# Performance work log

Measured on AMD Instinct MI355X. Metric: run time of the kernel, lower is better.

The kernel has to match this reference:

```python
import jax, jax.numpy as jnp
import numpy as np

N_NODES = 20000
N_EDGES = 320000
N_GRAPHS = 200
N_LAYERS = 2
TOWERS = 5
F_IN = 75        # divide_input=False -> each tower sees the full 75-dim input
F_OUT = 15       # out_channels // towers = 75 // 5
EDGE_DIM = 50
POST_IN = (4 * 3 + 1) * F_IN  # 4 aggregators * 3 scalers + self = 975
EPS_STD = 1e-5
EPS_BN = 1e-5


def setup_inputs() -> dict:
    key = jax.random.key(0)
    ks = jax.random.split(key, 16)
    x_idx = jax.random.randint(ks[0], (N_NODES,), 0, 10000)
    edge_index = jax.random.randint(ks[1], (2, N_EDGES), 0, N_NODES)
    edge_attr_idx = jax.random.randint(ks[2], (N_EDGES,), 0, 100)
    batch_idx = jnp.sort(jax.random.randint(ks[3], (N_NODES,), 0, N_GRAPHS))

    def g(k, shp, fan):
        return jax.random.normal(k, shp, jnp.float32) * np.float32(1.0 / np.sqrt(fan))

    inp = dict(
        x_idx=x_idx, edge_index=edge_index, edge_attr_idx=edge_attr_idx, batch_idx=batch_idx,
        node_emb=g(ks[4], (10000, F_IN), 1.0),
        edge_emb=g(ks[5], (100, EDGE_DIM), 1.0),
        W_edge=g(ks[6], (N_LAYERS, EDGE_DIM, F_IN), EDGE_DIM),
        b_edge=jnp.zeros((N_LAYERS, F_IN), jnp.float32),
        W_pre=g(ks[7], (N_LAYERS, TOWERS, 3 * F_IN, F_IN), 3 * F_IN),
        b_pre=jnp.zeros((N_LAYERS, TOWERS, F_IN), jnp.float32),
        W_post=g(ks[8], (N_LAYERS, TOWERS, POST_IN, F_OUT), POST_IN),
        b_post=jnp.zeros((N_LAYERS, TOWERS, F_OUT), jnp.float32),
        W_lin=g(ks[9], (N_LAYERS, F_IN, F_IN), F_IN),
        b_lin=jnp.zeros((N_LAYERS, F_IN), jnp.float32),
        bn_gamma=jnp.ones((N_LAYERS, F_IN), jnp.float32),
        bn_beta=jnp.zeros((N_LAYERS, F_IN), jnp.float32),
        W1=g(ks[10], (75, 50), 75), b1=jnp.zeros((50,), jnp.float32),
        W2=g(ks[11], (50, 25), 50), b2=jnp.zeros((25,), jnp.float32),
        W3=g(ks[12], (25, 1), 25), b3=jnp.zeros((1,), jnp.float32),
    )
    return inp


def reference(x_idx, edge_index, edge_attr_idx, batch_idx,
              node_emb, edge_emb, W_edge, b_edge, W_pre, b_pre,
              W_post, b_post, W_lin, b_lin, bn_gamma, bn_beta,
              W1, b1, W2, b2, W3, b3):
    src, dst = edge_index[0], edge_index[1]  # flow source_to_target: aggregate at dst
    x = node_emb[x_idx]                      # [N, 75]
    e_raw = edge_emb[edge_attr_idx]          # [E, 50]

    # in-degree based scalers (PNA); avg log-degree from this graph's degree histogram
    deg = jax.ops.segment_sum(jnp.ones((N_EDGES,), jnp.float32), dst, num_segments=N_NODES)
    avg_log = jnp.mean(jnp.log(deg + 1.0))
    deg_c = jnp.maximum(deg, 1.0)
    amp = (jnp.log(deg_c + 1.0) / avg_log)[:, None, None]
    att = (avg_log / jnp.log(deg_c + 1.0))[:, None, None]
    has_in = (deg > 0.0)[:, None, None]
    inv_deg = (1.0 / deg_c)[:, None, None]

    for l in range(N_LAYERS):
        # edge encoder (shared across towers)
        e = e_raw @ W_edge[l] + b_edge[l]                            # [E, 75]
        # message: since divide_input=False all towers see the same concat input
        h = jnp.concatenate([x[dst], x[src], e], axis=-1)            # [E, 225]
        m = jnp.einsum('ec,tcf->etf', h, W_pre[l]) + b_pre[l]        # [E, T, 75]
        # multi-aggregator reduction at dst
        mean = jax.ops.segment_sum(m, dst, num_segments=N_NODES) * inv_deg
        mean_sq = jax.ops.segment_sum(m * m, dst, num_segments=N_NODES) * inv_deg
        std = jnp.sqrt(jax.nn.relu(mean_sq - mean * mean) + EPS_STD)
        mn = jnp.where(has_in, jax.ops.segment_min(m, dst, num_segments=N_NODES), 0.0)
        mx = jnp.where(has_in, jax.ops.segment_max(m, dst, num_segments=N_NODES), 0.0)
        aggr = jnp.concatenate([mean, mn, mx, std], axis=-1)         # [N, T, 300]
        # degree scalers: identity, amplification, attenuation
        out = jnp.concatenate([aggr, aggr * amp, aggr * att], axis=-1)  # [N, T, 900]
        # update: concat self features, per-tower post MLP, then shared lin
        xt = jnp.broadcast_to(x[:, None, :], (N_NODES, TOWERS, F_IN))
        h2 = jnp.concatenate([xt, out], axis=-1)                     # [N, T, 975]
        y = jnp.einsum('ntc,tcf->ntf', h2, W_post[l]) + b_post[l]    # [N, T, 15]
        y = y.reshape(N_NODES, TOWERS * F_OUT) @ W_lin[l] + b_lin[l] # [N, 75]
        # BatchNorm (training-mode batch stats, biased variance) + ReLU
        mu = jnp.mean(y, axis=0)
        var = jnp.mean((y - mu) ** 2, axis=0)
        y = (y - mu) * jax.lax.rsqrt(var + EPS_BN) * bn_gamma[l] + bn_beta[l]
        x = jax.nn.relu(y)

    pooled = jax.ops.segment_sum(x, batch_idx, num_segments=N_GRAPHS)  # [G, 75]
    h = jax.nn.relu(pooled @ W1 + b1)
    h = jax.nn.relu(h @ W2 + b2)
    return h @ W3 + b3                                               # [G, 1]
```

## Files before the change

### kernel.cpp

```cpp
#include <hip/hip_runtime.h>
#include <hip/hip_bf16.h>
#include <math.h>

#define NN 20000
#define NE 320000
#define NG 200
#define FI 75
#define NT 5
#define FO 15
#define CH 375
#define PI 975
#define SMS 1608

typedef __attribute__((ext_vector_type(8))) short v8s;
typedef __attribute__((ext_vector_type(4))) float v4f;

__device__ __forceinline__ unsigned short f2bfu(float v) {
  __hip_bfloat16 h = __float2bfloat16(v);
  return *reinterpret_cast<unsigned short*>(&h);
}
__device__ __forceinline__ float uif(unsigned u) { return __uint_as_float(u); }

__global__ __launch_bounds__(256) void k_mega1(
    const int* __restrict__ xidx, const float* __restrict__ emb, float* __restrict__ x,
    const int* __restrict__ dstp, int* __restrict__ deg,
    const float* __restrict__ eemb, const float* __restrict__ W_edge,
    const float* __restrict__ b_edge, float* __restrict__ te,
    const float* __restrict__ W_pre, float* __restrict__ WAs,
    const float* __restrict__ W_post, float* __restrict__ V,
    const float* __restrict__ b_post, const float* __restrict__ W_lin,
    const float* __restrict__ b_lin, float* __restrict__ bc) {
  __shared__ float S[FI * 16];
  int b = blockIdx.x, tid = threadIdx.x;
  if (b < 5860) {
    int i = b * 256 + tid;
    if (i < NN * FI) {
      int n = i / FI, f = i - n * FI;
      x[i] = emb[xidx[n] * FI + f];
    }
  } else if (b < 7110) {
    int e = (b - 5860) * 256 + tid;
    if (e < NE) atomicAdd(&deg[dstp[e]], 1);
  } else if (b < 7310) {
    int la = b - 7110;
    int l = la / 100, a = la - l * 100;
    int f = tid;
    if (f < FI) {
      float acc = b_edge[l * FI + f];
      for (int j = 0; j < 50; ++j)
        acc = fmaf(eemb[a * 50 + j], W_edge[(l * 50 + j) * FI + f], acc);
      te[la * FI + f] = acc;
    }
  } else if (b < 7530) {
    int i = (b - 7310) * 256 + tid;
    if (i < 2 * FI * CH) {
      int c = i % CH;
      int k = (i / CH) % FI;
      int l = i / (CH * FI);
      int t = c / FI, f = c - t * FI;
      WAs[i] = W_pre[((size_t)(l * NT + t) * 225 + FI + k) * FI + f];
    }
  } else if (b < 7560) {
    int bid = b - 7530;
    int g = bid % 3;
    int lt = bid / 3;
    for (int idx = tid; idx < FI * 16; idx += 256) {
      int q = idx >> 4, f = idx & 15;
      float v = 0.f;
      if (f < FO) {
        const float* wb = W_post + (size_t)lt * PI * FO;
        int rowb = FI + g * 300 + q;
        v = wb[rowb * FO + f] + wb[(rowb + FI) * FO + f] + wb[(rowb + 2 * FI) * FO + f];
      }
      S[idx] = v;
    }
    __syncthreads();
    for (int idx = tid; idx < FI * 16; idx += 256) {
      int j = idx >> 4, f = idx & 15;
      float acc = 0.f;
      const float* wr = W_pre + ((size_t)lt * 225 + j) * FI;
      for (int q = 0; q < FI; ++q) acc = fmaf(wr[q], S[q * 16 + f], acc);
      V[((size_t)bid * FI + j) * 16 + f] = acc;
    }
  } else {
    int l = b - 7560;
    int g = tid;
    if (g < FI) {
      float acc = b_lin[l * FI + g];
      for (int j = 0; j < FI; ++j)
        acc = fmaf(b_post[l * FI + j], W_lin[(l * FI + j) * FI + g], acc);
      bc[l * 76 + g] = acc;
    }
  }
}

__global__ __launch_bounds__(1024) void k_mega2(
    const int* __restrict__ deg, int* __restrict__ off, int* __restrict__ cur,
    float* __restrict__ avglog,
    const float* __restrict__ te, const float* __restrict__ W_pre,
    const float* __restrict__ b_pre, unsigned short* __restrict__ tm,
    const float* __restrict__ W_post, const float* __restrict__ V,
    unsigned short* __restrict__ Bp,
    const float* __restrict__ WAs, unsigned short* __restrict__ Bxs,
    const float* __restrict__ W_lin, unsigned short* __restrict__ Blin) {
  __shared__ float red[1024];
  int b = blockIdx.x, t = threadIdx.x;
  if (b == 0) {
    int* wsum = (int*)red;
    int base = t * 20;
    int loc[20];
    int s = 0;
#pragma unroll
    for (int j = 0; j < 20; ++j) {
      int i = base + j;
      int v = (i < NN) ? deg[i] : 0;
      loc[j] = s;
      s += v;
    }
    int lane = t & 63, w = t >> 6;
    int inc = s;
    for (int o = 1; o < 64; o <<= 1) {
      int u = __shfl_up(inc, o, 64);
      if (lane >= o) inc += u;
    }
    if (lane == 63) wsum[w] = inc;
    __syncthreads();
    if (t == 0) {
      int a = 0;
#pragma unroll
      for (int k = 0; k < 16; ++k) { int v = wsum[k]; wsum[k] = a; a += v; }
    }
    __syncthreads();
    int tex = wsum[w] + inc - s;
#pragma unroll
    for (int j = 0; j < 20; ++j) {
      int i = base + j;
      if (i < NN) { int e = tex + loc[j]; off[i] = e; cur[i] = e; }
    }
    if (t == 1023) off[NN] = tex + s;
  } else if (b == 1) {
    float s = 0.f;
    for (int i = t; i < NN; i += 1024) s += logf((float)deg[i] + 1.f);
    red[t] = s;
    __syncthreads();
    for (int o = 512; o > 0; o >>= 1) {
      if (t < o) red[t] += red[t + o];
      __syncthreads();
    }
    if (t == 0) avglog[0] = red[0] / (float)NN;
  } else if (b < 77) {
    int idx = (b - 2) * 1024 + t;
    if (idx < 76800) {
      int la = idx / 384, c = idx - la * 384;
      int l = la / 100;
      float acc = 0.f;
      if (c < CH) {
        int tt = c / FI, f = c - tt * FI;
        acc = b_pre[(l * NT + tt) * FI + f];
        const float* ter = te + la * FI;
        for (int k = 0; k < FI; ++k)
          acc = fmaf(ter[k], W_pre[((size_t)(l * NT + tt) * 225 + 150 + k) * FI + f], acc);
      }
      tm[(size_t)la * 384 + c] = f2bfu(acc);
    }
  } else if (b < 302) {
    int i = (b - 77) * 1024 + t;
    if (i < 230400) {
      int j = i & 7;
      int lane = (i >> 3) & 63;
      int rem = i >> 9;
      int kb = rem % 15; rem /= 15;
      int g = rem % 3; rem /= 3;
      int tt = rem % 5;
      int l = rem / 5;
      int k = kb * 32 + (lane >> 4) * 8 + j;
      int f = lane & 15;
      float w = 0.f;
      if (f < FO) {
        int lt = l * NT + tt;
        if (k < 300) {
          int a = k / 75, ch = k - a * 75;
          w = W_post[((size_t)lt * PI + FI + g * 300 + a * 75 + ch) * FO + f];
        } else if (k >= 320 && k < 395) {
          w = V[(((size_t)(lt * 3 + g)) * FI + (k - 320)) * 16 + f];
        } else if (k >= 395 && k < 470 && g == 0) {
          w = W_post[((size_t)lt * PI + (k - 395)) * FO + f];
        }
      }
      Bp[i] = f2bfu(w);
    }
  } else if (b < 374) {
    int i = (b - 302) * 1024 + t;
    if (i < 73728) {
      int j = i & 7;
      int lane = (i >> 3) & 63;
      int rem = i >> 9;
      int nt = rem % 24; rem /= 24;
      int kb = rem % 3;
      int l = rem / 3;
      int k = kb * 32 + (lane >> 4) * 8 + j;
      int n = nt * 16 + (lane & 15);
      float w = 0.f;
      if (k < FI && n < CH) w = WAs[(size_t)l * FI * CH + k * CH + n];
      Bxs[i] = f2bfu(w);
    }
  } else {
    int i = (b - 374) * 1024 + t;
    if (i < 15360) {
      int j = i & 7;
      int lane = (i >> 3) & 63;
      int rem = i >> 9;
      int nt = rem % 5; rem /= 5;
      int kb = rem % 3;
      int l = rem / 3;
      int k = kb * 32 + (lane >> 4) * 8 + j;
      int f = nt * 16 + (lane & 15);
      float w = 0.f;
      if (k < FI && f < FI) w = W_lin[(size_t)l * FI * FI + k * FI + f];
      Blin[i] = f2bfu(w);
    }
  }
}

__global__ __launch_bounds__(256) void k_mega3(
    const int* __restrict__ srcp, const int* __restrict__ dstp,
    const int* __restrict__ attr, int* __restrict__ cur, int2* __restrict__ csr,
    const int* __restrict__ deg, const float* __restrict__ avglog,
    float* __restrict__ amp, float* __restrict__ att, float* __restrict__ inv) {
  int b = blockIdx.x, t = threadIdx.x;
  if (b < 1250) {
    int e = b * 256 + t;
    if (e < NE) {
      int pos = atomicAdd(&cur[dstp[e]], 1);
      csr[pos] = make_int2(srcp[e], attr[e]);
    }
  } else {
    int i = (b - 1250) * 256 + t;
    if (i < NN) {
      float dc = fmaxf((float)deg[i], 1.f);
      float ld = logf(dc + 1.f);
      float av = avglog[0];
      amp[i] = ld / av;
      att[i] = av / ld;
      inv[i] = 1.f / dc;
    }
  }
}

__global__ __launch_bounds__(256) void k_gemm_xs(const float* __restrict__ x,
                                                 const unsigned short* __restrict__ BxsL,
                                                 unsigned short* __restrict__ xsb,
                                                 const int* __restrict__ deg,
                                                 unsigned short* __restrict__ xh,
                                                 float* __restrict__ bnsum) {
  int tid = threadIdx.x;
  if (blockIdx.y == 1) {
    if (blockIdx.x == 0 && tid < 150) bnsum[tid] = 0.f;
    for (int i = blockIdx.x * 256 + tid; i < NN * 160; i += 625 * 256) {
      int r = i / 160, k = i - r * 160;
      float v = 0.f;
      if (k < FI) v = x[(size_t)r * FI + k] * ((deg[r] > 0) ? 1.f : 0.f);
      else if (k < 150) v = x[(size_t)r * FI + k - FI];
      xh[i] = f2bfu(v);
    }
    return;
  }
  __shared__ unsigned short As[32 * 104];
  __shared__ unsigned short Os[32 * 384];
  int m0 = blockIdx.x * 32;
  for (int i = tid; i < 32 * 104; i += 256) {
    int r = i / 104, k = i - r * 104;
    As[i] = (k < FI) ? f2bfu(x[(size_t)(m0 + r) * FI + k]) : 0;
  }
  __syncthreads();
  int lane = tid & 63, w = tid >> 6;
  int m16 = lane & 15, quad = lane >> 4;
  v4f acc0[6], acc1[6];
#pragma unroll
  for (int nt = 0; nt < 6; ++nt) {
    acc0[nt] = {0.f, 0.f, 0.f, 0.f};
    acc1[nt] = {0.f, 0.f, 0.f, 0.f};
  }
  const unsigned short* arow0 = As + m16 * 104 + quad * 8;
  const unsigned short* arow1 = As + (16 + m16) * 104 + quad * 8;
#pragma unroll
  for (int kb = 0; kb < 3; ++kb) {
    v8s a0 = *(const v8s*)(arow0 + kb * 32);
    v8s a1 = *(const v8s*)(arow1 + kb * 32);
#pragma unroll
    for (int nt = 0; nt < 6; ++nt) {
      v8s bf = *(const v8s*)(BxsL + ((size_t)(kb * 24 + w * 6 + nt) * 64 + lane) * 8);
      acc0[nt] = __builtin_amdgcn_mfma_f32_16x16x32_bf16(a0, bf, acc0[nt], 0, 0, 0);
      acc1[nt] = __builtin_amdgcn_mfma_f32_16x16x32_bf16(a1, bf, acc1[nt], 0, 0, 0);
    }
  }
#pragma unroll
  for (int nt = 0; nt < 6; ++nt) {
    int col = w * 96 + nt * 16 + m16;
#pragma unroll
    for (int r = 0; r < 4; ++r) {
      Os[(quad * 4 + r) * 384 + col] = f2bfu(acc0[nt][r]);
      Os[(16 + quad * 4 + r) * 384 + col] = f2bfu(acc1[nt][r]);
    }
  }
  __syncthreads();
  uint4* dst = (uint4*)(xsb + (size_t)m0 * 384);
  const uint4* src = (const uint4*)Os;
  for (int i = tid; i < 1536; i += 256) dst[i] = src[i];
}

__global__ __launch_bounds__(1024) void k_aggpost(
    const unsigned short* __restrict__ xs, const int2* __restrict__ csr,
    const int* __restrict__ off, const float* __restrict__ inv_deg,
    const unsigned short* __restrict__ tm, const unsigned short* __restrict__ xh,
    const unsigned short* __restrict__ Bp, const float* __restrict__ amp,
    const float* __restrict__ att, const unsigned short* __restrict__ BlinL,
    const float* __restrict__ bcL, float* __restrict__ yout,
    float* __restrict__ bnsum) {
  __shared__ __align__(16) unsigned short sm[16 * SMS];
  __shared__ __align__(16) unsigned short zs[16 * 96];
  __shared__ float ysum[FI], ysq[FI];
  int tid = threadIdx.x;
  int wv = tid >> 6, lane = tid & 63;
  int rel0 = blockIdx.x * 16;
  int n = rel0 + wv;
  if (tid < FI) { ysum[tid] = 0.f; ysq[tid] = 0.f; }
  for (int idx = tid; idx < 1600; idx += 1024) {
    int h = idx / 100, pp = idx - h * 100;
    int t = pp / 20, cc = pp - t * 20;
    sm[h * SMS + t * 320 + 300 + cc] = 0;
  }
  for (int i = tid; i < 16 * 21; i += 1024) {
    int r = i / 21, k = 75 + i - r * 21;
    zs[r * 96 + k] = 0;
  }
  if (n < NN) {
    int c0 = lane * 6;
    int o0 = off[n], o1 = off[n + 1];
    float s[6], q[6], mn[6], mx[6];
#pragma unroll
    for (int j = 0; j < 6; ++j) {
      s[j] = 0.f; q[j] = 0.f; mn[j] = INFINITY; mx[j] = -INFINITY;
    }
    auto proc = [&](uint3 xv, uint3 tv) {
      unsigned xa[3] = {xv.x, xv.y, xv.z};
      unsigned ta[3] = {tv.x, tv.y, tv.z};
#pragma unroll
      for (int j = 0; j < 3; ++j) {
        float z0 = uif(xa[j] << 16) + uif(ta[j] << 16);
        float z1 = uif(xa[j] & 0xffff0000u) + uif(ta[j] & 0xffff0000u);
        s[2 * j] += z0; q[2 * j] = fmaf(z0, z0, q[2 * j]);
        mn[2 * j] = fminf(mn[2 * j], z0); mx[2 * j] = fmaxf(mx[2 * j], z0);
        s[2 * j + 1] += z1; q[2 * j + 1] = fmaf(z1, z1, q[2 * j + 1]);
        mn[2 * j + 1] = fminf(mn[2 * j + 1], z1); mx[2 * j + 1] = fmaxf(mx[2 * j + 1], z1);
      }
    };
    int i = o0;
    for (; i + 4 <= o1; i += 4) {
      int2 e0 = csr[i], e1 = csr[i + 1], e2 = csr[i + 2], e3 = csr[i + 3];
      uint3 x0 = *(const uint3*)(xs + (size_t)e0.x * 384 + c0);
      uint3 t0 = *(const uint3*)(tm + (size_t)e0.y * 384 + c0);
      uint3 x1 = *(const uint3*)(xs + (size_t)e1.x * 384 + c0);
      uint3 t1 = *(const uint3*)(tm + (size_t)e1.y * 384 + c0);
      uint3 x2 = *(const uint3*)(xs + (size_t)e2.x * 384 + c0);
      uint3 t2 = *(const uint3*)(tm + (size_t)e2.y * 384 + c0);
      uint3 x3 = *(const uint3*)(xs + (size_t)e3.x * 384 + c0);
      uint3 t3 = *(const uint3*)(tm + (size_t)e3.y * 384 + c0);
      proc(x0, t0); proc(x1, t1); proc(x2, t2); proc(x3, t3);
    }
    for (; i < o1; ++i) {
      int2 e0 = csr[i];
      uint3 x0 = *(const uint3*)(xs + (size_t)e0.x * 384 + c0);
      uint3 t0 = *(const uint3*)(tm + (size_t)e0.y * 384 + c0);
      proc(x0, t0);
    }
    float inv = inv_deg[n];
    bool empty = (o1 == o0);
    unsigned short* srow = sm + wv * SMS;
#pragma unroll
    for (int j = 0; j < 6; ++j) {
      int c = c0 + j;
      if (c < CH) {
        float me = s[j] * inv;
        float sd = sqrtf(fmaxf(q[j] * inv - me * me, 0.f) + 1e-5f);
        float mnv = empty ? 0.f : mn[j];
        float mxv = empty ? 0.f : mx[j];
        int t = c / 75, ch = c - t * 75;
        unsigned short* bb = srow + t * 320;
        bb[ch] = f2bfu(me);
        bb[75 + ch] = f2bfu(mnv);
        bb[150 + ch] = f2bfu(mxv);
        bb[225 + ch] = f2bfu(sd);
      }
    }
  } else {
    uint* rowz = (uint*)(sm + wv * SMS);
    for (int idx2 = lane; idx2 < SMS / 2; idx2 += 64) rowz[idx2] = 0;
  }
  __syncthreads();
  int m16 = lane & 15, quad = lane >> 4;
  if (wv < NT) {
    int tw = wv;
    const unsigned short* arow = sm + m16 * SMS + tw * 320 + quad * 8;
    const unsigned short* xrow = xh + (size_t)(rel0 + m16) * 160 + quad * 8;
    const unsigned short* bp = Bp + ((size_t)tw * 3 * 15 * 64) * 8 + lane * 8;
    v4f a0 = {0.f, 0.f, 0.f, 0.f}, a1 = a0, a2 = a0;
#pragma unroll
    for (int kb = 0; kb < 15; ++kb) {
      v8s av = *(const v8s*)((kb < 10) ? (arow + kb * 32) : (xrow + (kb - 10) * 32));
      const unsigned short* bb = bp + (size_t)kb * 512;
      v8s b0 = *(const v8s*)(bb);
      v8s b1 = *(const v8s*)(bb + 15 * 512);
      v8s b2 = *(const v8s*)(bb + 30 * 512);
      a0 = __builtin_amdgcn_mfma_f32_16x16x32_bf16(av, b0, a0, 0, 0, 0);
      a1 = __builtin_amdgcn_mfma_f32_16x16x32_bf16(av, b1, a1, 0, 0, 0);
      a2 = __builtin_amdgcn_mfma_f32_16x16x32_bf16(av, b2, a2, 0, 0, 0);
    }
    int f = m16;
    if (f < FO) {
      int relZ = quad * 4;
#pragma unroll
      for (int r = 0; r < 4; ++r) {
        int nd = rel0 + relZ + r;
        int ndc = (nd < NN) ? nd : (NN - 1);
        float zz = a0[r] + amp[ndc] * a1[r] + att[ndc] * a2[r];
        zs[(relZ + r) * 96 + tw * FO + f] = f2bfu(zz);
      }
    }
  }
  __syncthreads();
  if (wv < NT) {
    int tw = wv;
    v4f acc2 = {0.f, 0.f, 0.f, 0.f};
#pragma unroll
    for (int kb = 0; kb < 3; ++kb) {
      v8s av = *(const v8s*)(zs + m16 * 96 + quad * 8 + kb * 32);
      v8s bl = *(const v8s*)(BlinL + ((size_t)(kb * 5 + tw) * 64 + lane) * 8);
      acc2 = __builtin_amdgcn_mfma_f32_16x16x32_bf16(av, bl, acc2, 0, 0, 0);
    }
    int fcol = tw * 16 + m16;
    if (fcol < FI) {
      float bcf = bcL[fcol];
      int nb = rel0 + quad * 4;
#pragma unroll
      for (int r = 0; r < 4; ++r) {
        int nd = nb + r;
        if (nd < NN) {
          float v = acc2[r] + bcf;
          yout[(size_t)nd * FI + fcol] = v;
          atomicAdd(&ysum[fcol], v);
          atomicAdd(&ysq[fcol], v * v);
        }
      }
    }
  }
  __syncthreads();
  if (tid < FI) {
    atomicAdd(&bnsum[tid], ysum[tid]);
    atomicAdd(&bnsum[FI + tid], ysq[tid]);
  }
}

__global__ __launch_bounds__(256) void k_bnfinapply(const float* __restrict__ y,
    const float* __restrict__ bnsum, const float* __restrict__ gamL,
    const float* __restrict__ betL, float* __restrict__ xo,
    const int* __restrict__ batch, float* __restrict__ pooled, int dopool) {
  __shared__ float sc[150];
  int tid = threadIdx.x;
  if (tid < FI) {
    float mu = bnsum[tid] / (float)NN;
    float var = bnsum[FI + tid] / (float)NN - mu * mu;
    float scl = gamL[tid] * rsqrtf(var + 1e-5f);
    sc[tid] = scl;
    sc[FI + tid] = betL[tid] - mu * scl;
  }
  if (!dopool) {
    for (int i = blockIdx.x * 256 + tid; i < NG * FI; i += gridDim.x * 256)
      pooled[i] = 0.f;
  }
  __syncthreads();
  int stride = gridDim.x * 256;
  for (int i = blockIdx.x * 256 + tid; i < NN * FI; i += stride) {
    int n = i / FI, f = i - n * FI;
    float v = fmaxf(fmaf(y[i], sc[f], sc[FI + f]), 0.f);
    xo[i] = v;
    if (dopool) atomicAdd(&pooled[batch[n] * FI + f], v);
  }
}

__global__ void k_head(const float* __restrict__ pooled, const float* __restrict__ W1,
                       const float* __restrict__ b1, const float* __restrict__ W2,
                       const float* __restrict__ b2, const float* __restrict__ W3,
                       const float* __restrict__ b3, float* __restrict__ out) {
  __shared__ float p[FI], h1[50], h2[25];
  int g = blockIdx.x, t = threadIdx.x;
  for (int i = t; i < FI; i += 64) p[i] = pooled[g * FI + i];
  __syncthreads();
  if (t < 50) {
    float a = b1[t];
    for (int j = 0; j < FI; ++j) a = fmaf(p[j], W1[j * 50 + t], a);
    h1[t] = fmaxf(a, 0.f);
  }
  __syncthreads();
  if (t < 25) {
    float a = b2[t];
    for (int j = 0; j < 50; ++j) a = fmaf(h1[j], W2[j * 25 + t], a);
    h2[t] = fmaxf(a, 0.f);
  }
  __syncthreads();
  if (t == 0) {
    float a = b3[0];
    for (int j = 0; j < 25; ++j) a = fmaf(h2[j], W3[j], a);
    out[g] = a;
  }
}

extern "C" void kernel_launch(void* const* d_in, const int* in_sizes, int n_in,
                              void* d_out, int out_size, void* d_ws, size_t ws_size,
                              hipStream_t stream) {
  const int* x_idx = (const int*)d_in[0];
  const int* eidx  = (const int*)d_in[1];
  const int* srcp  = eidx;
  const int* dstp  = eidx + NE;
  const int* eattr = (const int*)d_in[2];
  const int* batch = (const int*)d_in[3];
  const float* node_emb = (const float*)d_in[4];
  const float* edge_emb = (const float*)d_in[5];
  const float* W_edge = (const float*)d_in[6];
  const float* b_edge = (const float*)d_in[7];
  const float* W_pre  = (const float*)d_in[8];
  const float* b_pre  = (const float*)d_in[9];
  const float* W_post = (const float*)d_in[10];
  const float* b_post = (const float*)d_in[11];
  const float* W_lin  = (const float*)d_in[12];
  const float* b_lin  = (const float*)d_in[13];
  const float* gam = (const float*)d_in[14];
  const float* bet = (const float*)d_in[15];
  const float* W1 = (const float*)d_in[16];
  const float* b1 = (const float*)d_in[17];
  const float* W2 = (const float*)d_in[18];
  const float* b2 = (const float*)d_in[19];
  const float* W3 = (const float*)d_in[20];
  const float* b3 = (const float*)d_in[21];

  char* p = (char*)d_ws;
  auto alloc = [&](size_t b) -> char* {
    char* r = p;
    p += (b + 255) & ~(size_t)255;
    return r;
  };
  float* x_a   = (float*)alloc((size_t)NN * FI * 4);
  float* x_b   = (float*)alloc((size_t)NN * FI * 4);
  unsigned short* xs_bf = (unsigned short*)alloc((size_t)NN * 384 * 2);
  float* z     = (float*)alloc((size_t)NN * FI * 4);
  unsigned short* xh = (unsigned short*)alloc((size_t)(NN + 64) * 160 * 2);
  float* te    = (float*)alloc(2 * 100 * FI * 4);
  unsigned short* tm_bf = (unsigned short*)alloc((size_t)2 * 100 * 384 * 2);
  float* WAs   = (float*)alloc((size_t)2 * FI * CH * 4);
  float* V     = (float*)alloc((size_t)2 * NT * 3 * FI * 16 * 4);
  unsigned short* Bpk = (unsigned short*)alloc((size_t)230400 * 2);
  unsigned short* Bxs = (unsigned short*)alloc((size_t)73728 * 2);
  unsigned short* Blin = (unsigned short*)alloc((size_t)15360 * 2);
  float* bc    = (float*)alloc(2 * 76 * 4);
  float* ampv  = (float*)alloc((size_t)NN * 4);
  float* attv  = (float*)alloc((size_t)NN * 4);
  float* invv  = (float*)alloc((size_t)NN * 4);
  float* avglog = (float*)alloc(256);
  float* bnsum = (float*)alloc(2 * FI * 4);
  float* pooled = (float*)alloc((size_t)NG * FI * 4);
  int* deg = (int*)alloc((size_t)NN * 4);
  int* off = (int*)alloc((size_t)(NN + 1) * 4);
  int* cur = (int*)alloc((size_t)NN * 4);
  int2* csr = (int2*)alloc((size_t)NE * 8);

  hipMemsetAsync(deg, 0, (size_t)NN * 4, stream);

  k_mega1<<<7562, 256, 0, stream>>>(x_idx, node_emb, x_a, dstp, deg,
                                    edge_emb, W_edge, b_edge, te,
                                    W_pre, WAs, W_post, V,
                                    b_post, W_lin, b_lin, bc);
  k_mega2<<<389, 1024, 0, stream>>>(deg, off, cur, avglog,
                                    te, W_pre, b_pre, tm_bf, W_post, V, Bpk,
                                    WAs, Bxs, W_lin, Blin);
  k_mega3<<<1329, 256, 0, stream>>>(srcp, dstp, eattr, cur, csr,
                                    deg, avglog, ampv, attv, invv);

  for (int l = 0; l < 2; ++l) {
    const float* xin = (l == 0) ? x_a : x_b;
    float* xout = (l == 0) ? x_b : x_a;
    k_gemm_xs<<<dim3(625, 2), 256, 0, stream>>>(xin, Bxs + (size_t)l * 36864,
                                                xs_bf, deg, xh, bnsum);
    k_aggpost<<<1250, 1024, 0, stream>>>(xs_bf, csr, off, invv,
                                         tm_bf + (size_t)l * 100 * 384, xh,
                                         Bpk + (size_t)l * 115200, ampv, attv,
                                         Blin + (size_t)l * 7680, bc + l * 76,
                                         z, bnsum);
    k_bnfinapply<<<1250, 256, 0, stream>>>(z, bnsum, gam + l * FI, bet + l * FI,
                                           xout, batch, pooled, (l == 1) ? 1 : 0);
  }

  k_head<<<NG, 64, 0, stream>>>(pooled, W1, b1, W2, b2, W3, b3, (float*)d_out);
}
```

Measured before the change: 432.3 us.

## Sort nodes by descending degree to balance per-block aggregation work

Builds a degree histogram and a counting-sort permutation of nodes (highest degree first, capped at 63) in the setup kernels plus a new scan kernel. The aggregation/post kernel then processes nodes through this permutation, so the 16 wavefronts in each block handle nodes of similar degree and heavy blocks get scheduled first. This targets load imbalance where one high-degree node stalls a whole block. In exchange it adds an extra kernel launch and atomics, and makes the reads of xh, amp and att and the writes of yout scattered.

```diff
diff --git a/kernel.cpp b/kernel.cpp
--- a/kernel.cpp
+++ b/kernel.cpp
@@ -29,7 +29,8 @@
     const float* __restrict__ W_pre, float* __restrict__ WAs,
     const float* __restrict__ W_post, float* __restrict__ V,
     const float* __restrict__ b_post, const float* __restrict__ W_lin,
-    const float* __restrict__ b_lin, float* __restrict__ bc) {
+    const float* __restrict__ b_lin, float* __restrict__ bc,
+    int* __restrict__ hist2) {
   __shared__ float S[FI * 16];
   int b = blockIdx.x, tid = threadIdx.x;
   if (b < 5860) {
@@ -82,7 +83,7 @@
       for (int q = 0; q < FI; ++q) acc = fmaf(wr[q], S[q * 16 + f], acc);
       V[((size_t)bid * FI + j) * 16 + f] = acc;
     }
-  } else {
+  } else if (b < 7562) {
     int l = b - 7560;
     int g = tid;
     if (g < FI) {
@@ -91,6 +92,8 @@
         acc = fmaf(b_post[l * FI + j], W_lin[(l * FI + j) * FI + g], acc);
       bc[l * 76 + g] = acc;
     }
+  } else {
+    for (int i = tid; i < 1280; i += 256) hist2[i] = 0;
   }
 }
 
@@ -102,7 +105,8 @@
     const float* __restrict__ W_post, const float* __restrict__ V,
     unsigned short* __restrict__ Bp,
     const float* __restrict__ WAs, unsigned short* __restrict__ Bxs,
-    const float* __restrict__ W_lin, unsigned short* __restrict__ Blin) {
+    const float* __restrict__ W_lin, unsigned short* __restrict__ Blin,
+    int* __restrict__ hist2) {
   __shared__ float red[1024];
   int b = blockIdx.x, t = threadIdx.x;
   if (b == 0) {
@@ -204,7 +208,7 @@
       if (k < FI && n < CH) w = WAs[(size_t)l * FI * CH + k * CH + n];
       Bxs[i] = f2bfu(w);
     }
-  } else {
+  } else if (b < 389) {
     int i = (b - 374) * 1024 + t;
     if (i < 15360) {
       int j = i & 7;
@@ -219,6 +223,45 @@
       if (k < FI && f < FI) w = W_lin[(size_t)l * FI * FI + k * FI + f];
       Blin[i] = f2bfu(w);
     }
+  } else {
+    int* H = (int*)red;
+    if (t < 64) H[t] = 0;
+    __syncthreads();
+    int sl = b - 389;
+    int n = sl * 1024 + t;
+    if (n < NN) {
+      int d = deg[n];
+      if (d > 63) d = 63;
+      atomicAdd(&H[63 - d], 1);
+    }
+    __syncthreads();
+    if (t < 64) atomicAdd(&hist2[sl * 64 + t], H[t]);
+  }
+}
+
+__global__ __launch_bounds__(1024) void k_scan2(const int* __restrict__ hist2,
+                                                int* __restrict__ base2) {
+  __shared__ int H[1280];
+  __shared__ int TB[64];
+  int t = threadIdx.x;
+  for (int i = t; i < 1280; i += 1024) H[i] = hist2[i];
+  __syncthreads();
+  if (t < 64) {
+    int s = 0;
+    for (int sl = 0; sl < 20; ++sl) s += H[sl * 64 + t];
+    TB[t] = s;
+  }
+  __syncthreads();
+  if (t == 0) {
+    int a = 0;
+    for (int bn = 0; bn < 64; ++bn) { int v = TB[bn]; TB[bn] = a; a += v; }
+  }
+  __syncthreads();
+  for (int i = t; i < 1280; i += 1024) {
+    int sl = i >> 6, bn = i & 63;
+    int a = TB[bn];
+    for (int s2 = 0; s2 < sl; ++s2) a += H[s2 * 64 + bn];
+    base2[i] = a;
   }
 }
 
@@ -226,7 +269,8 @@
     const int* __restrict__ srcp, const int* __restrict__ dstp,
     const int* __restrict__ attr, int* __restrict__ cur, int2* __restrict__ csr,
     const int* __restrict__ deg, const float* __restrict__ avglog,
-    float* __restrict__ amp, float* __restrict__ att, float* __restrict__ inv) {
+    float* __restrict__ amp, float* __restrict__ att, float* __restrict__ inv,
+    int* __restrict__ base2, int* __restrict__ perm) {
   int b = blockIdx.x, t = threadIdx.x;
   if (b < 1250) {
     int e = b * 256 + t;
@@ -237,12 +281,16 @@
   } else {
     int i = (b - 1250) * 256 + t;
     if (i < NN) {
-      float dc = fmaxf((float)deg[i], 1.f);
+      int d = deg[i];
+      float dc = fmaxf((float)d, 1.f);
       float ld = logf(dc + 1.f);
       float av = avglog[0];
       amp[i] = ld / av;
       att[i] = av / ld;
       inv[i] = 1.f / dc;
+      int bin = (d > 63) ? 0 : (63 - d);
+      int pos = atomicAdd(&base2[(i >> 10) * 64 + bin], 1);
+      perm[pos] = i;
     }
   }
 }
@@ -316,14 +364,16 @@
     const unsigned short* __restrict__ Bp, const float* __restrict__ amp,
     const float* __restrict__ att, const unsigned short* __restrict__ BlinL,
     const float* __restrict__ bcL, float* __restrict__ yout,
-    float* __restrict__ bnsum) {
+    float* __restrict__ bnsum, const int* __restrict__ perm) {
   __shared__ __align__(16) unsigned short sm[16 * SMS];
   __shared__ __align__(16) unsigned short zs[16 * 96];
   __shared__ float ysum[FI], ysq[FI];
+  __shared__ int pids[16];
   int tid = threadIdx.x;
   int wv = tid >> 6, lane = tid & 63;
   int rel0 = blockIdx.x * 16;
-  int n = rel0 + wv;
+  int n = perm[rel0 + wv];
+  if (lane == 0) pids[wv] = n;
   if (tid < FI) { ysum[tid] = 0.f; ysq[tid] = 0.f; }
   for (int idx = tid; idx < 1600; idx += 1024) {
     int h = idx / 100, pp = idx - h * 100;
@@ -334,7 +384,7 @@
     int r = i / 21, k = 75 + i - r * 21;
     zs[r * 96 + k] = 0;
   }
-  if (n < NN) {
+  {
     int c0 = lane * 6;
     int o0 = off[n], o1 = off[n + 1];
     float s[6], q[6], mn[6], mx[6];
@@ -393,16 +443,13 @@
         bb[225 + ch] = f2bfu(sd);
       }
     }
-  } else {
-    uint* rowz = (uint*)(sm + wv * SMS);
-    for (int idx2 = lane; idx2 < SMS / 2; idx2 += 64) rowz[idx2] = 0;
   }
   __syncthreads();
   int m16 = lane & 15, quad = lane >> 4;
   if (wv < NT) {
     int tw = wv;
     const unsigned short* arow = sm + m16 * SMS + tw * 320 + quad * 8;
-    const unsigned short* xrow = xh + (size_t)(rel0 + m16) * 160 + quad * 8;
+    const unsigned short* xrow = xh + (size_t)pids[m16] * 160 + quad * 8;
     const unsigned short* bp = Bp + ((size_t)tw * 3 * 15 * 64) * 8 + lane * 8;
     v4f a0 = {0.f, 0.f, 0.f, 0.f}, a1 = a0, a2 = a0;
 #pragma unroll
@@ -421,9 +468,8 @@
       int relZ = quad * 4;
 #pragma unroll
       for (int r = 0; r < 4; ++r) {
-        int nd = rel0 + relZ + r;
-        int ndc = (nd < NN) ? nd : (NN - 1);
-        float zz = a0[r] + amp[ndc] * a1[r] + att[ndc] * a2[r];
+        int nd = pids[relZ + r];
+        float zz = a0[r] + amp[nd] * a1[r] + att[nd] * a2[r];
         zs[(relZ + r) * 96 + tw * FO + f] = f2bfu(zz);
       }
     }
@@ -441,16 +487,13 @@
     int fcol = tw * 16 + m16;
     if (fcol < FI) {
       float bcf = bcL[fcol];
-      int nb = rel0 + quad * 4;
 #pragma unroll
       for (int r = 0; r < 4; ++r) {
-        int nd = nb + r;
-        if (nd < NN) {
-          float v = acc2[r] + bcf;
-          yout[(size_t)nd * FI + fcol] = v;
-          atomicAdd(&ysum[fcol], v);
-          atomicAdd(&ysq[fcol], v * v);
-        }
+        int nd = pids[quad * 4 + r];
+        float v = acc2[r] + bcf;
+        yout[(size_t)nd * FI + fcol] = v;
+        atomicAdd(&ysum[fcol], v);
+        atomicAdd(&ysq[fcol], v * v);
       }
     }
   }
@@ -571,19 +614,23 @@
   int* deg = (int*)alloc((size_t)NN * 4);
   int* off = (int*)alloc((size_t)(NN + 1) * 4);
   int* cur = (int*)alloc((size_t)NN * 4);
+  int* hist2 = (int*)alloc(1280 * 4);
+  int* base2 = (int*)alloc(1280 * 4);
+  int* perm  = (int*)alloc((size_t)NN * 4);
   int2* csr = (int2*)alloc((size_t)NE * 8);
 
   hipMemsetAsync(deg, 0, (size_t)NN * 4, stream);
 
-  k_mega1<<<7562, 256, 0, stream>>>(x_idx, node_emb, x_a, dstp, deg,
+  k_mega1<<<7563, 256, 0, stream>>>(x_idx, node_emb, x_a, dstp, deg,
                                     edge_emb, W_edge, b_edge, te,
                                     W_pre, WAs, W_post, V,
-                                    b_post, W_lin, b_lin, bc);
-  k_mega2<<<389, 1024, 0, stream>>>(deg, off, cur, avglog,
+                                    b_post, W_lin, b_lin, bc, hist2);
+  k_mega2<<<409, 1024, 0, stream>>>(deg, off, cur, avglog,
                                     te, W_pre, b_pre, tm_bf, W_post, V, Bpk,
-                                    WAs, Bxs, W_lin, Blin);
+                                    WAs, Bxs, W_lin, Blin, hist2);
+  k_scan2<<<1, 1024, 0, stream>>>(hist2, base2);
   k_mega3<<<1329, 256, 0, stream>>>(srcp, dstp, eattr, cur, csr,
-                                    deg, avglog, ampv, attv, invv);
+                                    deg, avglog, ampv, attv, invv, base2, perm);
 
   for (int l = 0; l < 2; ++l) {
     const float* xin = (l == 0) ? x_a : x_b;
@@ -594,7 +641,7 @@
                                          tm_bf + (size_t)l * 100 * 384, xh,
                                          Bpk + (size_t)l * 115200, ampv, attv,
                                          Blin + (size_t)l * 7680, bc + l * 76,
-                                         z, bnsum);
+                                         z, bnsum, perm);
     k_bnfinapply<<<1250, 256, 0, stream>>>(z, bnsum, gam + l * FI, bet + l * FI,
                                            xout, batch, pooled, (l == 1) ? 1 : 0);
   }
```

After: 441.0 us. 2.0% more time.
